# Kernel tuning notes

Measured on AMD Instinct MI355X. Metric: run time of the kernel, lower is better.

The kernel has to match this reference:

```python
import jax, jax.numpy as jnp
import numpy as np

N = 50000   # nodes
E = 800000  # edges
F = 128     # feat_dim
I = 128     # internal_dim
G = 64      # graphs in batch
EPS = 1e-5


def setup_inputs() -> dict:
    key = jax.random.key(0)
    ks = jax.random.split(key, 32)
    s = 0.1
    inp = {
        'x': jax.random.normal(ks[0], (N, F), dtype=jnp.float32),
        'edge_index': jax.random.randint(ks[1], (2, E), 0, N, dtype=jnp.int64),
        'batch': jnp.sort(jax.random.randint(ks[2], (N,), 0, G, dtype=jnp.int64)),
        # InitialSubnet: Linear(F->I) + BN(I)
        'init_W': jax.random.normal(ks[3], (F, I)) * s,
        'init_b': jnp.zeros((I,)),
        'init_g': jnp.ones((I,)),
        'init_bt': jnp.zeros((I,)),
        # 2 middle EdgeConv subnets: Linear(2I->I) + BN(I)
        'mid_W': jax.random.normal(ks[4], (2, 2 * I, I)) * s,
        'mid_b': jnp.zeros((2, I)),
        'mid_g': jnp.ones((2, I)),
        'mid_bt': jnp.zeros((2, I)),
        # 1 er / 1 pr receptor-specific EdgeConv subnet each
        'er_W': jax.random.normal(ks[5], (1, 2 * I, I)) * s,
        'er_b': jnp.zeros((1, I)),
        'er_g': jnp.ones((1, I)),
        'er_bt': jnp.zeros((1, I)),
        'pr_W': jax.random.normal(ks[6], (1, 2 * I, I)) * s,
        'pr_b': jnp.zeros((1, I)),
        'pr_g': jnp.ones((1, I)),
        'pr_bt': jnp.zeros((1, I)),
        # 3 shared posts: Linear(I->2) + BN(2)
        'spost_W': jax.random.normal(ks[7], (3, I, 2)) * s,
        'spost_b': jnp.zeros((3, 2)),
        'spost_g': jnp.ones((3, 2)),
        'spost_bt': jnp.zeros((3, 2)),
        # 1 er post / 1 pr post: Linear(I->1) + BN(1)
        'erpost_W': jax.random.normal(ks[8], (1, I, 1)) * s,
        'erpost_b': jnp.zeros((1, 1)),
        'erpost_g': jnp.ones((1, 1)),
        'erpost_bt': jnp.zeros((1, 1)),
        'prpost_W': jax.random.normal(ks[9], (1, I, 1)) * s,
        'prpost_b': jnp.zeros((1, 1)),
        'prpost_g': jnp.ones((1, 1)),
        'prpost_bt': jnp.zeros((1, 1)),
    }
    return inp


def _bn(h, g, b):
    # BatchNorm1d in training mode: batch stats over the row dim, biased var
    m = jnp.mean(h, axis=0)
    v = jnp.var(h, axis=0)
    return (h - m) * jax.lax.rsqrt(v + EPS) * g + b


def _edgeconv(h, src, dst, W, b, g, bt):
    # PyG EdgeConv: msg = nn(cat([x_i, x_j - x_i])), aggr=max over incoming edges
    x_i = h[dst]                      # [E, I]
    x_j = h[src]                      # [E, I]
    msg = jnp.concatenate([x_i, x_j - x_i], axis=-1) @ W + b  # [E, I]
    msg = jax.nn.elu(_bn(msg, g, bt))
    out = jax.ops.segment_max(msg, dst, num_segments=N)
    return jnp.where(jnp.isneginf(out), 0.0, out)  # isolated nodes -> 0


def _post(h, batch, counts, W, b, g, bt):
    # elu(BN(Linear(h))) then global_mean_pool; dropout is identity (eval)
    h2 = jax.nn.elu(_bn(h @ W + b, g, bt))
    pooled = jax.ops.segment_sum(h2, batch, num_segments=G)
    return pooled / counts[:, None]


def reference(x, edge_index, batch,
              init_W, init_b, init_g, init_bt,
              mid_W, mid_b, mid_g, mid_bt,
              er_W, er_b, er_g, er_bt,
              pr_W, pr_b, pr_g, pr_bt,
              spost_W, spost_b, spost_g, spost_bt,
              erpost_W, erpost_b, erpost_g, erpost_bt,
              prpost_W, prpost_b, prpost_g, prpost_bt):
    src, dst = edge_index[0], edge_index[1]
    counts = jnp.maximum(jax.ops.segment_sum(jnp.ones((N,), x.dtype), batch, num_segments=G), 1.0)

    outs = []
    # InitialSubnet: gelu(BN(Linear(x)))
    h = jax.nn.gelu(_bn(x @ init_W + init_b, init_g, init_bt), approximate=False)
    outs.append(_post(h, batch, counts, spost_W[0], spost_b[0], spost_g[0], spost_bt[0]))

    for l in range(2):
        h = _edgeconv(h, src, dst, mid_W[l], mid_b[l], mid_g[l], mid_bt[l])
        outs.append(_post(h, batch, counts, spost_W[l + 1], spost_b[l + 1], spost_g[l + 1], spost_bt[l + 1]))

    er_h = h
    pr_h = h
    for l in range(1):
        er_h = _edgeconv(er_h, src, dst, er_W[l], er_b[l], er_g[l], er_bt[l])
        er_out = _post(er_h, batch, counts, erpost_W[l], erpost_b[l], erpost_g[l], erpost_bt[l])
        pr_h = _edgeconv(pr_h, src, dst, pr_W[l], pr_b[l], pr_g[l], pr_bt[l])
        pr_out = _post(pr_h, batch, counts, prpost_W[l], prpost_b[l], prpost_g[l], prpost_bt[l])
        outs.append(jnp.concatenate([er_out, pr_out], axis=-1))

    agg = outs[0]
    for o in outs[1:]:
        agg = agg + o
    return agg  # [G, 2]
```

## Files before the change

### kernel.cpp

```cpp
#include <hip/hip_runtime.h>
#include <math.h>

#define EPS 1e-5f

typedef float f32x4v __attribute__((ext_vector_type(4)));
typedef short s16x8  __attribute__((ext_vector_type(8)));

__device__ __forceinline__ float elu_f(float x) { return x > 0.f ? x : expm1f(x); }
__device__ __forceinline__ float blo(unsigned u) { return __uint_as_float(u << 16); }
__device__ __forceinline__ float bhi(unsigned u) { return __uint_as_float(u & 0xffff0000u); }
__device__ __forceinline__ unsigned f2b(float f) {
  unsigned u = __float_as_uint(f);
  unsigned r = ((u >> 16) & 1u) + 0x7fffu;
  return (u + r) >> 16;
}
__device__ __forceinline__ unsigned pack2(float a, float b) {
  return f2b(a) | (f2b(b) << 16);
}

__global__ __launch_bounds__(256) void prep_csr0(const float* __restrict__ init_W,
    const float* __restrict__ mid_W, const float* __restrict__ er_W,
    const float* __restrict__ pr_W, const float* __restrict__ mid_g,
    const float* __restrict__ er_g, const float* __restrict__ pr_g,
    unsigned short* __restrict__ WT,
    const int* __restrict__ dst, int* __restrict__ partials, int Ecnt,
    const int* __restrict__ batch, float* __restrict__ counts, int Nn) {
  if (blockIdx.x < 320) {
    int grp = blockIdx.x >> 6;
    int i = (blockIdx.x & 63) * 256 + threadIdx.x;
    if (i >= 16384) return;
    int k = i >> 7, c = i & 127;
    if (grp == 0) {
      WT[c * 128 + k] = (unsigned short)f2b(init_W[k * 128 + c]);
      return;
    }
    const float* W; const float* g; unsigned short* Wd; unsigned short* W2;
    if (grp == 1)      { W = mid_W;             g = mid_g;       Wd = WT + 1 * 16384; W2 = WT + 2 * 16384; }
    else if (grp == 2) { W = mid_W + 256 * 128; g = mid_g + 128; Wd = WT + 3 * 16384; W2 = WT + 4 * 16384; }
    else if (grp == 3) { W = er_W;              g = er_g;        Wd = WT + 5 * 16384; W2 = WT + 6 * 16384; }
    else               { W = pr_W;              g = pr_g;        Wd = WT + 7 * 16384; W2 = WT + 8 * 16384; }
    float sg = (g[c] >= 0.f) ? 1.f : -1.f;
    float w1 = W[k * 128 + c];
    float w2 = W[(k + 128) * 128 + c];
    Wd[c * 128 + k] = (unsigned short)f2b((w1 - w2) * sg);
    W2[c * 128 + k] = (unsigned short)f2b(w2 * sg);
  } else {
    int b = blockIdx.x - 320;
    if (b < 64) {
      __shared__ int cnt[256];
      cnt[threadIdx.x] = 0;
      __syncthreads();
      int i0 = b * 256 + threadIdx.x, stride = 64 * 256;
      for (int e = i0; e < Ecnt; e += stride) atomicAdd(&cnt[(unsigned)dst[e] >> 8], 1);
      __syncthreads();
      partials[b * 256 + threadIdx.x] = cnt[threadIdx.x];
    } else {
      __shared__ float lc[64];
      if (threadIdx.x < 64) lc[threadIdx.x] = 0.f;
      __syncthreads();
      int i0 = (b - 64) * 256 + threadIdx.x, stride = 64 * 256;
      for (int n = i0; n < Nn; n += stride) atomicAdd(&lc[batch[n]], 1.f);
      __syncthreads();
      if (threadIdx.x < 64 && lc[threadIdx.x] != 0.f)
        atomicAdd(&counts[threadIdx.x * 16], lc[threadIdx.x]);
    }
  }
}

__global__ __launch_bounds__(256) void csr_p0_scan(const int* __restrict__ partials,
    int nblk, int* __restrict__ bucket_base, int* __restrict__ gcursor) {
  __shared__ int sc[256];
  int b = threadIdx.x;
  int s = 0;
  for (int k = 0; k < nblk; ++k) s += partials[k * 256 + b];
  sc[b] = s;
  __syncthreads();
  for (int off = 1; off < 256; off <<= 1) {
    int t = (b >= off) ? sc[b - off] : 0;
    __syncthreads();
    sc[b] += t;
    __syncthreads();
  }
  int excl = sc[b] - s;
  bucket_base[b] = excl;
  gcursor[b * 16] = excl;
  if (b == 255) bucket_base[256] = sc[255];
}

#define P1_CHUNK 4096
__global__ __launch_bounds__(256) void csr_p1_bin(const int* __restrict__ src,
    const int* __restrict__ dst, int* __restrict__ gcursor,
    unsigned* __restrict__ binned, int Ecnt) {
  __shared__ unsigned stage[P1_CHUNK];
  __shared__ int cnt[256], lbase[256], gbase[256], lcur[256], sc[256];
  int tid = threadIdx.x;
  int e0 = blockIdx.x * P1_CHUNK;
  int ecnt = Ecnt - e0; if (ecnt > P1_CHUNK) ecnt = P1_CHUNK;
  cnt[tid] = 0;
  __syncthreads();
  for (int i = tid; i < ecnt; i += 256) atomicAdd(&cnt[(unsigned)dst[e0 + i] >> 8], 1);
  __syncthreads();
  sc[tid] = cnt[tid];
  __syncthreads();
  for (int off = 1; off < 256; off <<= 1) {
    int t = (tid >= off) ? sc[tid - off] : 0;
    __syncthreads();
    sc[tid] += t;
    __syncthreads();
  }
  lbase[tid] = sc[tid] - cnt[tid];
  lcur[tid] = lbase[tid];
  gbase[tid] = (cnt[tid] > 0) ? atomicAdd(&gcursor[tid * 16], cnt[tid]) : 0;
  __syncthreads();
  for (int i = tid; i < ecnt; i += 256) {
    int d = dst[e0 + i], s = src[e0 + i];
    int bk = (unsigned)d >> 8;
    int p = atomicAdd(&lcur[bk], 1);
    stage[p] = ((unsigned)bk << 24) | ((unsigned)(d & 255) << 16) | (unsigned)s;
  }
  __syncthreads();
  for (int i = tid; i < ecnt; i += 256) {
    unsigned v = stage[i];
    int bk = v >> 24;
    binned[gbase[bk] + (i - lbase[bk])] = v;
  }
}

#define P2_CAP 12288
__global__ __launch_bounds__(256) void csr_p2_sort(const unsigned* __restrict__ binned,
    const int* __restrict__ bucket_base, unsigned short* __restrict__ csr_src,
    int* __restrict__ deg, int* __restrict__ rowstart, int Nn) {
  __shared__ unsigned short stage[P2_CAP];
  __shared__ int cnt[256], lbase[256], lcur[256], sc[256];
  int b = blockIdx.x, tid = threadIdx.x;
  int base = bucket_base[b];
  int bcnt = bucket_base[b + 1] - base;
  if (bcnt > P2_CAP) bcnt = P2_CAP;
  cnt[tid] = 0;
  __syncthreads();
  for (int i = tid; i < bcnt; i += 256) atomicAdd(&cnt[(binned[base + i] >> 16) & 255], 1);
  __syncthreads();
  sc[tid] = cnt[tid];
  __syncthreads();
  for (int off = 1; off < 256; off <<= 1) {
    int t = (tid >= off) ? sc[tid - off] : 0;
    __syncthreads();
    sc[tid] += t;
    __syncthreads();
  }
  lbase[tid] = sc[tid] - cnt[tid];
  lcur[tid] = lbase[tid];
  int node = b * 256 + tid;
  if (node < Nn) { deg[node] = cnt[tid]; rowstart[node] = base + lbase[tid]; }
  __syncthreads();
  for (int i = tid; i < bcnt; i += 256) {
    unsigned v = binned[base + i];
    int j = (v >> 16) & 255;
    int p = atomicAdd(&lcur[j], 1);
    stage[p] = (unsigned short)(v & 0xffffu);
  }
  __syncthreads();
  for (int i = tid; i < bcnt; i += 256) csr_src[base + i] = stage[i];
}

template<int XF32, int NMAT, int STATS>
__global__ __launch_bounds__(256, 3) void gemm_mfma(const void* __restrict__ Xv,
    const unsigned short* __restrict__ W0t, const unsigned short* __restrict__ W1t,
    const unsigned short* __restrict__ W2t, const unsigned short* __restrict__ W3t,
    unsigned short* __restrict__ Y0, unsigned short* __restrict__ Y1,
    unsigned short* __restrict__ Y2, unsigned short* __restrict__ Y3,
    float* __restrict__ stOut, int Nrows) {
  int tid = threadIdx.x, lane = tid & 63, wv = tid >> 6;
  int r0 = blockIdx.x * 64;
  int rlo = lane & 15, kg = lane >> 4;
  s16x8 zf = {0, 0, 0, 0, 0, 0, 0, 0};
  s16x8 af[4][4];
#pragma unroll
  for (int rg = 0; rg < 4; ++rg) {
    int arow = r0 + rg * 16 + rlo;
    if (arow < Nrows) {
      if (XF32) {
        const float* xr = (const float*)Xv + (size_t)arow * 128 + kg * 8;
#pragma unroll
        for (int s2 = 0; s2 < 4; ++s2) {
          float4 a = *(const float4*)(xr + s2 * 32);
          float4 b = *(const float4*)(xr + s2 * 32 + 4);
          s16x8 t;
          t[0] = (short)f2b(a.x); t[1] = (short)f2b(a.y);
          t[2] = (short)f2b(a.z); t[3] = (short)f2b(a.w);
          t[4] = (short)f2b(b.x); t[5] = (short)f2b(b.y);
          t[6] = (short)f2b(b.z); t[7] = (short)f2b(b.w);
          af[rg][s2] = t;
        }
      } else {
        const unsigned short* xr = (const unsigned short*)Xv + (size_t)arow * 128 + kg * 8;
#pragma unroll
        for (int s2 = 0; s2 < 4; ++s2) af[rg][s2] = *(const s16x8*)(xr + s2 * 32);
      }
    } else {
#pragma unroll
      for (int s2 = 0; s2 < 4; ++s2) af[rg][s2] = zf;
    }
  }
  const unsigned short* Ws[4] = {W0t, W1t, W2t, W3t};
  unsigned short* Ys[4] = {Y0, Y1, Y2, Y3};
#pragma unroll
  for (int o = 0; o < NMAT; ++o) {
    const unsigned short* Wt = Ws[o];
    unsigned short* Y = Ys[o];
#pragma unroll
    for (int t = 0; t < 2; ++t) {
      int nt = wv * 2 + t;
      const unsigned short* wp = Wt + (size_t)(nt * 16 + rlo) * 128 + kg * 8;
      s16x8 wf[4];
#pragma unroll
      for (int s2 = 0; s2 < 4; ++s2) wf[s2] = *(const s16x8*)(wp + s2 * 32);
      f32x4v acc[4];
#pragma unroll
      for (int rg = 0; rg < 4; ++rg) acc[rg] = (f32x4v){0.f, 0.f, 0.f, 0.f};
#pragma unroll
      for (int s2 = 0; s2 < 4; ++s2)
#pragma unroll
        for (int rg = 0; rg < 4; ++rg)
          acc[rg] = __builtin_amdgcn_mfma_f32_16x16x32_bf16(wf[s2], af[rg][s2], acc[rg], 0, 0, 0);
      float ps0 = 0.f, ps1 = 0.f, ps2 = 0.f, ps3 = 0.f;
      float pq0 = 0.f, pq1 = 0.f, pq2 = 0.f, pq3 = 0.f;
#pragma unroll
      for (int rg = 0; rg < 4; ++rg) {
        int arow = r0 + rg * 16 + rlo;
        if (arow < Nrows) {
          uint2 ov;
          ov.x = pack2(acc[rg][0], acc[rg][1]);
          ov.y = pack2(acc[rg][2], acc[rg][3]);
          *(uint2*)(Y + (size_t)arow * 128 + nt * 16 + kg * 4) = ov;
          if (STATS) {
            float y0 = blo(ov.x), y1 = bhi(ov.x), y2 = blo(ov.y), y3 = bhi(ov.y);
            ps0 += y0; pq0 += y0 * y0;
            ps1 += y1; pq1 += y1 * y1;
            ps2 += y2; pq2 += y2 * y2;
            ps3 += y3; pq3 += y3 * y3;
          }
        }
      }
      if (STATS) {
#pragma unroll
        for (int off = 1; off < 16; off <<= 1) {
          ps0 += __shfl_xor(ps0, off); pq0 += __shfl_xor(pq0, off);
          ps1 += __shfl_xor(ps1, off); pq1 += __shfl_xor(pq1, off);
          ps2 += __shfl_xor(ps2, off); pq2 += __shfl_xor(pq2, off);
          ps3 += __shfl_xor(ps3, off); pq3 += __shfl_xor(pq3, off);
        }
        if (rlo == 0) {
          int col = nt * 16 + kg * 4;
          float* sb = stOut + (size_t)(blockIdx.x & 15) * 256;
          atomicAdd(&sb[2 * col + 0], ps0); atomicAdd(&sb[2 * col + 1], pq0);
          atomicAdd(&sb[2 * (col + 1)], ps1); atomicAdd(&sb[2 * (col + 1) + 1], pq1);
          atomicAdd(&sb[2 * (col + 2)], ps2); atomicAdd(&sb[2 * (col + 2) + 1], pq2);
          atomicAdd(&sb[2 * (col + 3)], ps3); atomicAdd(&sb[2 * (col + 3) + 1], pq3);
        }
      }
    }
  }
}

__global__ __launch_bounds__(256, 8) void conv_pass(const unsigned short* __restrict__ A,
    const unsigned short* __restrict__ B, const unsigned short* __restrict__ csr_src,
    const int* __restrict__ rowstart, const int* __restrict__ deg,
    const float* __restrict__ g, unsigned short* __restrict__ Mx,
    float* __restrict__ st, int Nn, int convBlks,
    const float* __restrict__ zPp, const int* __restrict__ batch,
    const float* __restrict__ counts, const float* __restrict__ stpp,
    const float* __restrict__ g2, const float* __restrict__ bt2,
    float* __restrict__ out, float invN) {
  __shared__ float s_sum[128], s_ssq[128];
  int tid = threadIdx.x;
  if ((int)blockIdx.x >= convBlks) {
    __shared__ float lacc[128];
    if (tid < 128) lacc[tid] = 0.f;
    __syncthreads();
    float m0 = stpp[0] * invN, v0 = stpp[128] * invN - m0 * m0;
    float scale0 = g2[0] * rsqrtf(v0 + EPS), shift0 = bt2[0] - m0 * scale0;
    float m1 = stpp[64] * invN, v1 = stpp[192] * invN - m1 * m1;
    float scale1 = g2[1] * rsqrtf(v1 + EPS), shift1 = bt2[1] - m1 * scale1;
    int i0 = (blockIdx.x - convBlks) * 256 + tid;
    int stride = 32 * 256;
    for (int n = i0; n < Nn; n += stride) {
      int gi = batch[n];
      atomicAdd(&lacc[gi * 2], elu_f(zPp[n * 2] * scale0 + shift0));
      atomicAdd(&lacc[gi * 2 + 1], elu_f(zPp[n * 2 + 1] * scale1 + shift1));
    }
    __syncthreads();
    if (tid < 128) {
      int gi = tid >> 1, p = tid & 1;
      float v = lacc[tid];
      if (v != 0.f) atomicAdd(&out[gi * 2 + p], v / fmaxf(counts[gi * 16], 1.f));
    }
    return;
  }
  if (tid < 128) { s_sum[tid] = 0.f; s_ssq[tid] = 0.f; }
  __syncthreads();
  int lane = tid & 63;
  int wave = __builtin_amdgcn_readfirstlane((blockIdx.x << 2) + (tid >> 6));
  int wstride = convBlks << 2;
  int c0 = lane * 2;
  float sg0 = (g[c0] >= 0.f) ? 1.f : -1.f;
  float sg1 = (g[c0 + 1] >= 0.f) ? 1.f : -1.f;
  const unsigned* A32 = (const unsigned*)A;
  const unsigned* B32 = (const unsigned*)B;
  unsigned* M32 = (unsigned*)Mx;
  float s0 = 0.f, ss0 = 0.f, s1 = 0.f, ss1 = 0.f;
  for (int n = wave; n < Nn; n += wstride) {
    int dg = deg[n];
    if (dg == 0) continue;
    int beg = rowstart[n];
    unsigned ua = A32[(size_t)n * 64 + lane];
    float a0 = blo(ua), a1 = bhi(ua);
    float mx0 = -INFINITY, mx1 = -INFINITY;
    int e = beg, eend = beg + dg;
    for (; e + 8 <= eend; e += 8) {
      int idx[8];
#pragma unroll
      for (int q = 0; q < 8; ++q) idx[q] = csr_src[e + q];
      unsigned uu[8];
#pragma unroll
      for (int q = 0; q < 8; ++q) uu[q] = B32[(size_t)idx[q] * 64 + lane];
#pragma unroll
      for (int q = 0; q < 8; ++q) {
        float m0 = a0 + blo(uu[q]), m1 = a1 + bhi(uu[q]);
        s0 += m0; ss0 += m0 * m0;
        s1 += m1; ss1 += m1 * m1;
        mx0 = fmaxf(mx0, m0);
        mx1 = fmaxf(mx1, m1);
      }
    }
    for (; e + 2 <= eend; e += 2) {
      int ia = csr_src[e], ib = csr_src[e + 1];
      unsigned u0 = B32[(size_t)ia * 64 + lane];
      unsigned u1 = B32[(size_t)ib * 64 + lane];
      float m00 = a0 + blo(u0), m01 = a1 + bhi(u0);
      float m10 = a0 + blo(u1), m11 = a1 + bhi(u1);
      s0 += m00 + m10; ss0 += m00 * m00 + m10 * m10;
      s1 += m01 + m11; ss1 += m01 * m01 + m11 * m11;
      mx0 = fmaxf(mx0, fmaxf(m00, m10));
      mx1 = fmaxf(mx1, fmaxf(m01, m11));
    }
    if (e < eend) {
      unsigned u0 = B32[(size_t)csr_src[e] * 64 + lane];
      float m00 = a0 + blo(u0), m01 = a1 + bhi(u0);
      s0 += m00; ss0 += m00 * m00;
      s1 += m01; ss1 += m01 * m01;
      mx0 = fmaxf(mx0, m00);
      mx1 = fmaxf(mx1, m01);
    }
    M32[(size_t)n * 64 + lane] = pack2(mx0, mx1);
  }
  atomicAdd(&s_sum[c0], s0 * sg0); atomicAdd(&s_ssq[c0], ss0);
  atomicAdd(&s_sum[c0 + 1], s1 * sg1); atomicAdd(&s_ssq[c0 + 1], ss1);
  __syncthreads();
  if (tid < 128) {
    float* sb = st + (size_t)(blockIdx.x & 15) * 256;
    atomicAdd(&sb[2 * tid], s_sum[tid]);
    atomicAdd(&sb[2 * tid + 1], s_ssq[tid]);
  }
}

__global__ __launch_bounds__(256, 8) void conv_pass_dual(
    const unsigned short* __restrict__ Aer, const unsigned short* __restrict__ Ber,
    const unsigned short* __restrict__ Apr, const unsigned short* __restrict__ Bpr,
    const unsigned short* __restrict__ csr_src,
    const int* __restrict__ rowstart, const int* __restrict__ deg,
    const float* __restrict__ g_er, const float* __restrict__ g_pr,
    unsigned short* __restrict__ Mer, unsigned short* __restrict__ Mpr,
    float* __restrict__ st_er, float* __restrict__ st_pr, int Nn, int convBlks,
    const float* __restrict__ zPp, const int* __restrict__ batch,
    const float* __restrict__ counts, const float* __restrict__ stpp,
    const float* __restrict__ g2, const float* __restrict__ bt2,
    float* __restrict__ out, float invN) {
  __shared__ float s_e[256], s_p[256];
  int tid = threadIdx.x;
  if ((int)blockIdx.x >= convBlks) {
    __shared__ float lacc[128];
    if (tid < 128) lacc[tid] = 0.f;
    __syncthreads();
    float m0 = stpp[0] * invN, v0 = stpp[128] * invN - m0 * m0;
    float scale0 = g2[0] * rsqrtf(v0 + EPS), shift0 = bt2[0] - m0 * scale0;
    float m1 = stpp[64] * invN, v1 = stpp[192] * invN - m1 * m1;
    float scale1 = g2[1] * rsqrtf(v1 + EPS), shift1 = bt2[1] - m1 * scale1;
    int i0 = (blockIdx.x - convBlks) * 256 + tid;
    int stride = 32 * 256;
    for (int n = i0; n < Nn; n += stride) {
      int gi = batch[n];
      atomicAdd(&lacc[gi * 2], elu_f(zPp[n * 2] * scale0 + shift0));
      atomicAdd(&lacc[gi * 2 + 1], elu_f(zPp[n * 2 + 1] * scale1 + shift1));
    }
    __syncthreads();
    if (tid < 128) {
      int gi = tid >> 1, p = tid & 1;
      float v = lacc[tid];
      if (v != 0.f) atomicAdd(&out[gi * 2 + p], v / fmaxf(counts[gi * 16], 1.f));
    }
    return;
  }
  s_e[tid] = 0.f; s_p[tid] = 0.f;
  __syncthreads();
  int lane = tid & 63;
  int wave = __builtin_amdgcn_readfirstlane((blockIdx.x << 2) + (tid >> 6));
  int wstride = convBlks << 2;
  int c0 = lane * 2;
  float sge0 = (g_er[c0] >= 0.f) ? 1.f : -1.f;
  float sge1 = (g_er[c0 + 1] >= 0.f) ? 1.f : -1.f;
  float sgp0 = (g_pr[c0] >= 0.f) ? 1.f : -1.f;
  float sgp1 = (g_pr[c0 + 1] >= 0.f) ? 1.f : -1.f;
  const unsigned* Ae32 = (const unsigned*)Aer;
  const unsigned* Be32 = (const unsigned*)Ber;
  const unsigned* Ap32 = (const unsigned*)Apr;
  const unsigned* Bp32 = (const unsigned*)Bpr;
  unsigned* Me32 = (unsigned*)Mer;
  unsigned* Mp32 = (unsigned*)Mpr;
  float se0 = 0.f, sse0 = 0.f, se1 = 0.f, sse1 = 0.f;
  float sp0 = 0.f, ssp0 = 0.f, sp1 = 0.f, ssp1 = 0.f;
  for (int n = wave; n < Nn; n += wstride) {
    int dg = deg[n];
    if (dg == 0) continue;
    int beg = rowstart[n];
    unsigned uae = Ae32[(size_t)n * 64 + lane];
    unsigned uap = Ap32[(size_t)n * 64 + lane];
    float ae0 = blo(uae), ae1 = bhi(uae);
    float ap0 = blo(uap), ap1 = bhi(uap);
    float mxe0 = -INFINITY, mxe1 = -INFINITY, mxp0 = -INFINITY, mxp1 = -INFINITY;
    int e = beg, eend = beg + dg;
    for (; e + 8 <= eend; e += 8) {
      int idx[8];
#pragma unroll
      for (int q = 0; q < 8; ++q) idx[q] = csr_src[e + q];
      unsigned ue[8], up[8];
#pragma unroll
      for (int q = 0; q < 8; ++q) ue[q] = Be32[(size_t)idx[q] * 64 + lane];
#pragma unroll
      for (int q = 0; q < 8; ++q) up[q] = Bp32[(size_t)idx[q] * 64 + lane];
#pragma unroll
      for (int q = 0; q < 8; ++q) {
        float me0 = ae0 + blo(ue[q]), me1 = ae1 + bhi(ue[q]);
        float mp0 = ap0 + blo(up[q]), mp1 = ap1 + bhi(up[q]);
        se0 += me0; sse0 += me0 * me0; se1 += me1; sse1 += me1 * me1;
        sp0 += mp0; ssp0 += mp0 * mp0; sp1 += mp1; ssp1 += mp1 * mp1;
        mxe0 = fmaxf(mxe0, me0); mxe1 = fmaxf(mxe1, me1);
        mxp0 = fmaxf(mxp0, mp0); mxp1 = fmaxf(mxp1, mp1);
      }
    }
    for (; e + 2 <= eend; e += 2) {
      int i0 = csr_src[e], i1 = csr_src[e + 1];
      unsigned ue0 = Be32[(size_t)i0 * 64 + lane];
      unsigned up0 = Bp32[(size_t)i0 * 64 + lane];
      unsigned ue1 = Be32[(size_t)i1 * 64 + lane];
      unsigned up1 = Bp32[(size_t)i1 * 64 + lane];
      float me0 = ae0 + blo(ue0), me1 = ae1 + bhi(ue0);
      float mp0 = ap0 + blo(up0), mp1 = ap1 + bhi(up0);
      float ne0 = ae0 + blo(ue1), ne1 = ae1 + bhi(ue1);
      float np0 = ap0 + blo(up1), np1 = ap1 + bhi(up1);
      se0 += me0 + ne0; sse0 += me0 * me0 + ne0 * ne0;
      se1 += me1 + ne1; sse1 += me1 * me1 + ne1 * ne1;
      sp0 += mp0 + np0; ssp0 += mp0 * mp0 + np0 * np0;
      sp1 += mp1 + np1; ssp1 += mp1 * mp1 + np1 * np1;
      mxe0 = fmaxf(mxe0, fmaxf(me0, ne0)); mxe1 = fmaxf(mxe1, fmaxf(me1, ne1));
      mxp0 = fmaxf(mxp0, fmaxf(mp0, np0)); mxp1 = fmaxf(mxp1, fmaxf(mp1, np1));
    }
    if (e < eend) {
      int i0 = csr_src[e];
      unsigned ue = Be32[(size_t)i0 * 64 + lane];
      unsigned up = Bp32[(size_t)i0 * 64 + lane];
      float me0 = ae0 + blo(ue), me1 = ae1 + bhi(ue);
      float mp0 = ap0 + blo(up), mp1 = ap1 + bhi(up);
      se0 += me0; sse0 += me0 * me0; se1 += me1; sse1 += me1 * me1;
      sp0 += mp0; ssp0 += mp0 * mp0; sp1 += mp1; ssp1 += mp1 * mp1;
      mxe0 = fmaxf(mxe0, me0); mxe1 = fmaxf(mxe1, me1);
      mxp0 = fmaxf(mxp0, mp0); mxp1 = fmaxf(mxp1, mp1);
    }
    Me32[(size_t)n * 64 + lane] = pack2(mxe0, mxe1);
    Mp32[(size_t)n * 64 + lane] = pack2(mxp0, mxp1);
  }
  atomicAdd(&s_e[2 * c0], se0 * sge0);       atomicAdd(&s_e[2 * c0 + 1], sse0);
  atomicAdd(&s_e[2 * (c0 + 1)], se1 * sge1); atomicAdd(&s_e[2 * (c0 + 1) + 1], sse1);
  atomicAdd(&s_p[2 * c0], sp0 * sgp0);       atomicAdd(&s_p[2 * c0 + 1], ssp0);
  atomicAdd(&s_p[2 * (c0 + 1)], sp1 * sgp1); atomicAdd(&s_p[2 * (c0 + 1) + 1], ssp1);
  __syncthreads();
  {
    float* se = st_er + (size_t)(blockIdx.x & 15) * 256;
    float* sp = st_pr + (size_t)(blockIdx.x & 15) * 256;
    atomicAdd(&se[tid], s_e[tid]);
    atomicAdd(&sp[tid], s_p[tid]);
  }
}

template<int MODE>
__global__ __launch_bounds__(256) void fused_post16(const unsigned short* __restrict__ Zb,
    const int* __restrict__ deg, const float* __restrict__ stn,
    const float* __restrict__ g, const float* __restrict__ bt,
    const float* __restrict__ Wp, unsigned short* __restrict__ Hb,
    float* __restrict__ zP, float* __restrict__ stp, int Nn, float invCnt, int P) {
  __shared__ float lscale[128], lshift[128];
  __shared__ float red[4][4];
  int tid = threadIdx.x;
  if (tid < 128) {
    float sm = 0.f, sq = 0.f;
#pragma unroll
    for (int k = 0; k < 16; ++k) {
      sm += stn[k * 256 + 2 * tid];
      sq += stn[k * 256 + 2 * tid + 1];
    }
    float mean = sm * invCnt;
    float var = sq * invCnt - mean * mean;
    float sc = g[tid] * rsqrtf(var + EPS);
    float sh = bt[tid] - mean * sc;
    if (MODE == 1 && g[tid] < 0.f) sc = -sc;
    lscale[tid] = sc; lshift[tid] = sh;
  }
  __syncthreads();
  int sub = tid & 15, c0 = sub * 8;
  float sc[8], sh[8], w0[8], w1[8];
#pragma unroll
  for (int j = 0; j < 8; ++j) {
    sc[j] = lscale[c0 + j]; sh[j] = lshift[c0 + j];
    w0[j] = Wp[(c0 + j) * P];
    w1[j] = (P > 1) ? Wp[(c0 + j) * P + 1] : 0.f;
  }
  int g0 = (blockIdx.x * 256 + tid) >> 4;
  int gstride = gridDim.x * 16;
  bool leader = (sub == 0);
  float s0 = 0.f, ss0 = 0.f, s1 = 0.f, ss1 = 0.f;
  for (int n = g0; n < Nn; n += gstride) {
    float d0 = 0.f, d1 = 0.f;
    unsigned ow[4];
    bool live = (MODE == 0) || (deg[n] > 0);
    if (live) {
      uint4 v = ((const uint4*)(Zb + (size_t)n * 128))[sub];
      unsigned w[4] = {v.x, v.y, v.z, v.w};
#pragma unroll
      for (int u = 0; u < 4; ++u) {
        float t0 = blo(w[u]) * sc[2 * u] + sh[2 * u];
        float t1 = bhi(w[u]) * sc[2 * u + 1] + sh[2 * u + 1];
        float y0, y1;
        if (MODE == 0) {
          y0 = 0.5f * t0 * (1.f + erff(t0 * 0.70710678118f));
          y1 = 0.5f * t1 * (1.f + erff(t1 * 0.70710678118f));
        } else {
          y0 = elu_f(t0); y1 = elu_f(t1);
        }
        d0 += y0 * w0[2 * u] + y1 * w0[2 * u + 1];
        d1 += y0 * w1[2 * u] + y1 * w1[2 * u + 1];
        ow[u] = pack2(y0, y1);
      }
    } else {
      ow[0] = ow[1] = ow[2] = ow[3] = 0u;
    }
    if (Hb) ((uint4*)(Hb + (size_t)n * 128))[sub] = make_uint4(ow[0], ow[1], ow[2], ow[3]);
#pragma unroll
    for (int off = 1; off < 16; off <<= 1) {
      d0 += __shfl_xor(d0, off);
      d1 += __shfl_xor(d1, off);
    }
    if (leader) {
      zP[n * 2] = d0;
      if (P > 1) zP[n * 2 + 1] = d1;
      s0 += d0; ss0 += d0 * d0; s1 += d1; ss1 += d1 * d1;
    }
  }
  s0 += __shfl_xor(s0, 16);  s0 += __shfl_xor(s0, 32);
  s1 += __shfl_xor(s1, 16);  s1 += __shfl_xor(s1, 32);
  ss0 += __shfl_xor(ss0, 16); ss0 += __shfl_xor(ss0, 32);
  ss1 += __shfl_xor(ss1, 16); ss1 += __shfl_xor(ss1, 32);
  int wv = tid >> 6;
  if ((tid & 63) == 0) { red[wv][0] = s0; red[wv][1] = s1; red[wv][2] = ss0; red[wv][3] = ss1; }
  __syncthreads();
  if (tid < 4) {
    float v = red[0][tid] + red[1][tid] + red[2][tid] + red[3][tid];
    atomicAdd(&stp[tid * 64], v);
  }
}

__global__ __launch_bounds__(256) void fused_post16_dual(
    const unsigned short* __restrict__ Mer, const unsigned short* __restrict__ Mpr,
    const int* __restrict__ deg,
    const float* __restrict__ st_er, const float* __restrict__ st_pr,
    const float* __restrict__ g_er, const float* __restrict__ bt_er,
    const float* __restrict__ g_pr, const float* __restrict__ bt_pr,
    const float* __restrict__ Wer, const float* __restrict__ Wpr,
    float* __restrict__ zP, float* __restrict__ stp_er, float* __restrict__ stp_pr,
    int Nn, float invE) {
  __shared__ float sce_l[128], she_l[128], scp_l[128], shp_l[128];
  __shared__ float red[4][4];
  int tid = threadIdx.x;
  if (tid < 128) {
    float sme = 0.f, sqe = 0.f, smp = 0.f, sqp = 0.f;
#pragma unroll
    for (int k = 0; k < 16; ++k) {
      sme += st_er[k * 256 + 2 * tid];
      sqe += st_er[k * 256 + 2 * tid + 1];
      smp += st_pr[k * 256 + 2 * tid];
      sqp += st_pr[k * 256 + 2 * tid + 1];
    }
    float mean = sme * invE;
    float var = sqe * invE - mean * mean;
    float sc = g_er[tid] * rsqrtf(var + EPS);
    she_l[tid] = bt_er[tid] - mean * sc;
    sce_l[tid] = (g_er[tid] < 0.f) ? -sc : sc;
    mean = smp * invE;
    var = sqp * invE - mean * mean;
    sc = g_pr[tid] * rsqrtf(var + EPS);
    shp_l[tid] = bt_pr[tid] - mean * sc;
    scp_l[tid] = (g_pr[tid] < 0.f) ? -sc : sc;
  }
  __syncthreads();
  int sub = tid & 15, c0 = sub * 8;
  float sce[8], she[8], scp[8], shp[8], we[8], wp[8];
#pragma unroll
  for (int j = 0; j < 8; ++j) {
    sce[j] = sce_l[c0 + j]; she[j] = she_l[c0 + j];
    scp[j] = scp_l[c0 + j]; shp[j] = shp_l[c0 + j];
    we[j] = Wer[c0 + j]; wp[j] = Wpr[c0 + j];
  }
  int g0 = (blockIdx.x * 256 + tid) >> 4;
  int gstride = gridDim.x * 16;
  bool leader = (sub == 0);
  float s0 = 0.f, ss0 = 0.f, s1 = 0.f, ss1 = 0.f;
  for (int n = g0; n < Nn; n += gstride) {
    float d0 = 0.f, d1 = 0.f;
    if (deg[n] > 0) {
      uint4 ve = ((const uint4*)(Mer + (size_t)n * 128))[sub];
      uint4 vp = ((const uint4*)(Mpr + (size_t)n * 128))[sub];
      unsigned wea[4] = {ve.x, ve.y, ve.z, ve.w};
      unsigned wpa[4] = {vp.x, vp.y, vp.z, vp.w};
#pragma unroll
      for (int u = 0; u < 4; ++u) {
        float te0 = blo(wea[u]) * sce[2 * u] + she[2 * u];
        float te1 = bhi(wea[u]) * sce[2 * u + 1] + she[2 * u + 1];
        float tp0 = blo(wpa[u]) * scp[2 * u] + shp[2 * u];
        float tp1 = bhi(wpa[u]) * scp[2 * u + 1] + shp[2 * u + 1];
        d0 += elu_f(te0) * we[2 * u] + elu_f(te1) * we[2 * u + 1];
        d1 += elu_f(tp0) * wp[2 * u] + elu_f(tp1) * wp[2 * u + 1];
      }
    }
#pragma unroll
    for (int off = 1; off < 16; off <<= 1) {
      d0 += __shfl_xor(d0, off);
      d1 += __shfl_xor(d1, off);
    }
    if (leader) {
      zP[n * 2] = d0;
      zP[n * 2 + 1] = d1;
      s0 += d0; ss0 += d0 * d0; s1 += d1; ss1 += d1 * d1;
    }
  }
  s0 += __shfl_xor(s0, 16);  s0 += __shfl_xor(s0, 32);
  s1 += __shfl_xor(s1, 16);  s1 += __shfl_xor(s1, 32);
  ss0 += __shfl_xor(ss0, 16); ss0 += __shfl_xor(ss0, 32);
  ss1 += __shfl_xor(ss1, 16); ss1 += __shfl_xor(ss1, 32);
  int wv = tid >> 6;
  if ((tid & 63) == 0) { red[wv][0] = s0; red[wv][1] = s1; red[wv][2] = ss0; red[wv][3] = ss1; }
  __syncthreads();
  if (tid < 4) {
    float v = red[0][tid] + red[1][tid] + red[2][tid] + red[3][tid];
    if (tid == 0) atomicAdd(&stp_er[0], v);
    else if (tid == 1) atomicAdd(&stp_pr[0], v);
    else if (tid == 2) atomicAdd(&stp_er[128], v);
    else atomicAdd(&stp_pr[128], v);
  }
}

__global__ __launch_bounds__(256) void post_phase2_dual(const float* __restrict__ zP,
    const int* __restrict__ batch, const float* __restrict__ counts,
    const float* __restrict__ st_er, const float* __restrict__ st_pr,
    const float* __restrict__ g_er, const float* __restrict__ bt_er,
    const float* __restrict__ g_pr, const float* __restrict__ bt_pr,
    float* __restrict__ out, int Nrows, float invN) {
  __shared__ float lacc[128];
  if (threadIdx.x < 128) lacc[threadIdx.x] = 0.f;
  __syncthreads();
  float m0 = st_er[0] * invN;
  float v0 = st_er[128] * invN - m0 * m0;
  float scale0 = g_er[0] * rsqrtf(v0 + EPS);
  float shift0 = bt_er[0] - m0 * scale0;
  float m1 = st_pr[0] * invN;
  float v1 = st_pr[128] * invN - m1 * m1;
  float scale1 = g_pr[0] * rsqrtf(v1 + EPS);
  float shift1 = bt_pr[0] - m1 * scale1;
  int i0 = blockIdx.x * 256 + threadIdx.x;
  int stride = gridDim.x * 256;
  for (int n = i0; n < Nrows; n += stride) {
    int gi = batch[n];
    float y0 = elu_f(zP[n * 2] * scale0 + shift0);
    float y1 = elu_f(zP[n * 2 + 1] * scale1 + shift1);
    atomicAdd(&lacc[gi * 2], y0);
    atomicAdd(&lacc[gi * 2 + 1], y1);
  }
  __syncthreads();
  if (threadIdx.x < 128) {
    int gi = threadIdx.x >> 1, p = threadIdx.x & 1;
    float v = lacc[threadIdx.x];
    if (v != 0.f)
      atomicAdd(&out[gi * 2 + p], v / fmaxf(counts[gi * 16], 1.f));
  }
}

extern "C" void kernel_launch(void* const* d_in, const int* in_sizes, int n_in,
                              void* d_out, int out_size, void* d_ws, size_t ws_size,
                              hipStream_t stream) {
  const float* x       = (const float*)d_in[0];
  const int*   ei      = (const int*)d_in[1];
  const int*   batch   = (const int*)d_in[2];
  const float* init_W  = (const float*)d_in[3];
  const float* init_g  = (const float*)d_in[5];
  const float* init_bt = (const float*)d_in[6];
  const float* mid_W   = (const float*)d_in[7];
  const float* mid_g   = (const float*)d_in[9];
  const float* mid_bt  = (const float*)d_in[10];
  const float* er_W    = (const float*)d_in[11];
  const float* er_g    = (const float*)d_in[13];
  const float* er_bt   = (const float*)d_in[14];
  const float* pr_W    = (const float*)d_in[15];
  const float* pr_g    = (const float*)d_in[17];
  const float* pr_bt   = (const float*)d_in[18];
  const float* spost_W  = (const float*)d_in[19];
  const float* spost_g  = (const float*)d_in[21];
  const float* spost_bt = (const float*)d_in[22];
  const float* erpost_W  = (const float*)d_in[23];
  const float* erpost_g  = (const float*)d_in[25];
  const float* erpost_bt = (const float*)d_in[26];
  const float* prpost_W  = (const float*)d_in[27];
  const float* prpost_g  = (const float*)d_in[29];
  const float* prpost_bt = (const float*)d_in[30];

  int N = in_sizes[0] / 128;
  int E = in_sizes[1] / 2;
  float invN = 1.f / (float)N;
  float invE = 1.f / (float)E;
  float* out = (float*)d_out;

  const int CONV_BLKS = 2048;
  int nbuck = (N + 255) >> 8;

  size_t NB = (size_t)N * 128;
  unsigned short* Hb  = (unsigned short*)d_ws;
  unsigned short* Tb0 = Hb + NB;
  unsigned short* Tb1 = Tb0 + NB;
  unsigned short* Tb2 = Tb1 + NB;
  unsigned short* Tb3 = Tb2 + NB;
  unsigned short* MxB = Tb3 + NB;
  unsigned short* MxB2 = MxB + NB;
  float* zP     = (float*)(MxB2 + NB);
  float* counts = zP + (size_t)2 * N;
  float* stats  = counts + 1024;
  float* post   = stats + 5 * 4096;
  unsigned short* WT = (unsigned short*)(post + 5 * 512);
  int* deg        = (int*)(WT + 9 * 16384);
  int* rowstart   = deg + N;
  int* bucketbase = rowstart + N;
  int* gcursor    = bucketbase + 320;
  int* partials   = gcursor + 256 * 16;
  unsigned* binned = (unsigned*)(partials + 64 * 256);
  unsigned short* csr_src = (unsigned short*)(binned + E);

  int gemmGrid = (N + 63) / 64;

  hipMemsetAsync(d_out, 0, out_size * sizeof(float), stream);
  hipMemsetAsync(counts, 0, (1024 + 5 * 4096 + 5 * 512) * sizeof(float), stream);

  const int* e_src = ei;
  const int* e_dst = ei + E;
  prep_csr0<<<448, 256, 0, stream>>>(init_W, mid_W, er_W, pr_W, mid_g, er_g, pr_g, WT,
                                     e_dst, partials, E, batch, counts, N);
  csr_p0_scan<<<1, 256, 0, stream>>>(partials, 64, bucketbase, gcursor);
  csr_p1_bin<<<(E + P1_CHUNK - 1) / P1_CHUNK, 256, 0, stream>>>(e_src, e_dst, gcursor, binned, E);
  csr_p2_sort<<<nbuck, 256, 0, stream>>>(binned, bucketbase, csr_src, deg, rowstart, N);

  gemm_mfma<1, 1, 1><<<gemmGrid, 256, 0, stream>>>((const void*)x, WT, nullptr, nullptr, nullptr,
                                                   Tb0, nullptr, nullptr, nullptr, stats, N);
  fused_post16<0><<<512, 256, 0, stream>>>(Tb0, deg, stats, init_g, init_bt, spost_W,
                                           Hb, zP, post + 0 * 512, N, invN, 2);

  gemm_mfma<0, 2, 0><<<gemmGrid, 256, 0, stream>>>((const void*)Hb,
      WT + 1 * 16384, WT + 2 * 16384, nullptr, nullptr, Tb0, Tb1, nullptr, nullptr, nullptr, N);
  conv_pass<<<CONV_BLKS + 32, 256, 0, stream>>>(Tb0, Tb1, csr_src, rowstart, deg, mid_g,
      MxB, stats + 1 * 4096, N, CONV_BLKS,
      zP, batch, counts, post + 0 * 512, spost_g, spost_bt, out, invN);
  fused_post16<1><<<512, 256, 0, stream>>>(MxB, deg, stats + 1 * 4096, mid_g, mid_bt,
                                           spost_W + 256, Hb, zP, post + 1 * 512, N, invE, 2);

  gemm_mfma<0, 2, 0><<<gemmGrid, 256, 0, stream>>>((const void*)Hb,
      WT + 3 * 16384, WT + 4 * 16384, nullptr, nullptr, Tb0, Tb1, nullptr, nullptr, nullptr, N);
  conv_pass<<<CONV_BLKS + 32, 256, 0, stream>>>(Tb0, Tb1, csr_src, rowstart, deg, mid_g + 128,
      MxB, stats + 2 * 4096, N, CONV_BLKS,
      zP, batch, counts, post + 1 * 512, spost_g + 2, spost_bt + 2, out, invN);
  fused_post16<1><<<512, 256, 0, stream>>>(MxB, deg, stats + 2 * 4096, mid_g + 128, mid_bt + 128,
                                           spost_W + 512, Hb, zP, post + 2 * 512, N, invE, 2);

  gemm_mfma<0, 4, 0><<<gemmGrid, 256, 0, stream>>>((const void*)Hb,
      WT + 5 * 16384, WT + 6 * 16384, WT + 7 * 16384, WT + 8 * 16384,
      Tb0, Tb1, Tb2, Tb3, nullptr, N);
  conv_pass_dual<<<CONV_BLKS + 32, 256, 0, stream>>>(Tb0, Tb1, Tb2, Tb3, csr_src, rowstart, deg,
      er_g, pr_g, MxB, MxB2, stats + 3 * 4096, stats + 4 * 4096, N, CONV_BLKS,
      zP, batch, counts, post + 2 * 512, spost_g + 4, spost_bt + 4, out, invN);

  fused_post16_dual<<<512, 256, 0, stream>>>(MxB, MxB2, deg,
      stats + 3 * 4096, stats + 4 * 4096, er_g, er_bt, pr_g, pr_bt,
      erpost_W, prpost_W, zP, post + 3 * 512, post + 4 * 512, N, invE);
  post_phase2_dual<<<32, 256, 0, stream>>>(zP, batch, counts,
      post + 3 * 512, post + 4 * 512, erpost_g, erpost_bt, prpost_g, prpost_bt,
      out, N, invN);
}
```

Baseline: 419.8 us.

## Fuse BN+activation+post projection into the following MFMA GEMM prologue

Replaces the separate fused_post16 kernels and the following gemm_mfma with a single gemm_act kernel. It applies batch-norm, GELU/ELU and the post projection to each 64-row tile in shared memory, then runs the MFMA matmuls from LDS. The goal is to drop the write and re-read of the intermediate activation buffer Hb and to save kernel launches. In exchange, each GEMM block now does the activation work, and launch_bounds(256,3) with the larger LDS use may reduce occupancy.

New measurement: 385.5 us. 8.2% less time.

```diff
diff --git a/kernel.cpp b/kernel.cpp
--- a/kernel.cpp
+++ b/kernel.cpp
@@ -263,6 +263,133 @@
   }
 }
 
+template<int NMAT, int ACT>
+__global__ __launch_bounds__(256, 3) void gemm_act(const unsigned short* __restrict__ Xv,
+    const unsigned short* __restrict__ W0t, const unsigned short* __restrict__ W1t,
+    const unsigned short* __restrict__ W2t, const unsigned short* __restrict__ W3t,
+    unsigned short* __restrict__ Y0, unsigned short* __restrict__ Y1,
+    unsigned short* __restrict__ Y2, unsigned short* __restrict__ Y3,
+    const float* __restrict__ stn, const float* __restrict__ g,
+    const float* __restrict__ bt, const int* __restrict__ deg,
+    const float* __restrict__ Wp, float* __restrict__ zP, float* __restrict__ stp,
+    float invCnt, int Nrows) {
+  __shared__ unsigned short hl[64][136];
+  __shared__ float lsc[128], lsh[128], lw0[128], lw1[128];
+  __shared__ float red[4][4];
+  int tid = threadIdx.x, lane = tid & 63, wv = tid >> 6;
+  int r0 = blockIdx.x * 64;
+  int rlo = lane & 15, kg = lane >> 4;
+  if (tid < 128) {
+    float sm = 0.f, sq = 0.f;
+#pragma unroll
+    for (int k = 0; k < 16; ++k) {
+      sm += stn[k * 256 + 2 * tid];
+      sq += stn[k * 256 + 2 * tid + 1];
+    }
+    float mean = sm * invCnt;
+    float var = sq * invCnt - mean * mean;
+    float sc = g[tid] * rsqrtf(var + EPS);
+    float sh = bt[tid] - mean * sc;
+    if (ACT == 2 && g[tid] < 0.f) sc = -sc;
+    lsc[tid] = sc; lsh[tid] = sh;
+    lw0[tid] = Wp[tid * 2]; lw1[tid] = Wp[tid * 2 + 1];
+  }
+  __syncthreads();
+  {
+    int row = tid >> 2, q = tid & 3;
+    int arow = r0 + row;
+    bool rok = arow < Nrows;
+    int lrow = rok ? arow : 0;
+    float live = 1.f;
+    if (ACT == 2) live = (rok && deg[arow] > 0) ? 1.f : 0.f;
+    else live = rok ? 1.f : 0.f;
+    const uint4* xr = (const uint4*)(Xv + (size_t)lrow * 128 + q * 32);
+    float dd0 = 0.f, dd1 = 0.f;
+#pragma unroll
+    for (int b = 0; b < 4; ++b) {
+      uint4 v = xr[b];
+      unsigned w[4] = {v.x, v.y, v.z, v.w};
+      int cb = q * 32 + b * 8;
+#pragma unroll
+      for (int u = 0; u < 4; ++u) {
+        int c = cb + 2 * u;
+        float t0 = blo(w[u]) * lsc[c] + lsh[c];
+        float t1 = bhi(w[u]) * lsc[c + 1] + lsh[c + 1];
+        float y0, y1;
+        if (ACT == 1) {
+          y0 = 0.5f * t0 * (1.f + erff(t0 * 0.70710678118f));
+          y1 = 0.5f * t1 * (1.f + erff(t1 * 0.70710678118f));
+        } else {
+          y0 = elu_f(t0); y1 = elu_f(t1);
+        }
+        y0 *= live; y1 *= live;
+        *(unsigned*)&hl[row][c] = pack2(y0, y1);
+        dd0 += y0 * lw0[c] + y1 * lw0[c + 1];
+        dd1 += y0 * lw1[c] + y1 * lw1[c + 1];
+      }
+    }
+    dd0 += __shfl_xor(dd0, 1); dd0 += __shfl_xor(dd0, 2);
+    dd1 += __shfl_xor(dd1, 1); dd1 += __shfl_xor(dd1, 2);
+    if (q == 0 && rok) {
+      zP[(size_t)arow * 2] = dd0;
+      zP[(size_t)arow * 2 + 1] = dd1;
+    }
+    float s0v = (q == 0 && rok) ? dd0 : 0.f;
+    float s1v = (q == 0 && rok) ? dd1 : 0.f;
+    float q0v = s0v * s0v, q1v = s1v * s1v;
+#pragma unroll
+    for (int off = 4; off < 64; off <<= 1) {
+      s0v += __shfl_xor(s0v, off); s1v += __shfl_xor(s1v, off);
+      q0v += __shfl_xor(q0v, off); q1v += __shfl_xor(q1v, off);
+    }
+    if (lane == 0) { red[wv][0] = s0v; red[wv][1] = s1v; red[wv][2] = q0v; red[wv][3] = q1v; }
+  }
+  __syncthreads();
+  if (tid < 4) {
+    float v = red[0][tid] + red[1][tid] + red[2][tid] + red[3][tid];
+    atomicAdd(&stp[tid * 64], v);
+  }
+  s16x8 af[4][4];
+#pragma unroll
+  for (int rg = 0; rg < 4; ++rg)
+#pragma unroll
+    for (int s2 = 0; s2 < 4; ++s2)
+      af[rg][s2] = *(const s16x8*)&hl[rg * 16 + rlo][kg * 8 + s2 * 32];
+  const unsigned short* Ws[4] = {W0t, W1t, W2t, W3t};
+  unsigned short* Ys[4] = {Y0, Y1, Y2, Y3};
+#pragma unroll
+  for (int o = 0; o < NMAT; ++o) {
+    const unsigned short* Wt = Ws[o];
+    unsigned short* Y = Ys[o];
+#pragma unroll
+    for (int t = 0; t < 2; ++t) {
+      int nt = wv * 2 + t;
+      const unsigned short* wp = Wt + (size_t)(nt * 16 + rlo) * 128 + kg * 8;
+      s16x8 wf[4];
+#pragma unroll
+      for (int s2 = 0; s2 < 4; ++s2) wf[s2] = *(const s16x8*)(wp + s2 * 32);
+      f32x4v acc[4];
+#pragma unroll
+      for (int rg = 0; rg < 4; ++rg) acc[rg] = (f32x4v){0.f, 0.f, 0.f, 0.f};
+#pragma unroll
+      for (int s2 = 0; s2 < 4; ++s2)
+#pragma unroll
+        for (int rg = 0; rg < 4; ++rg)
+          acc[rg] = __builtin_amdgcn_mfma_f32_16x16x32_bf16(wf[s2], af[rg][s2], acc[rg], 0, 0, 0);
+#pragma unroll
+      for (int rg = 0; rg < 4; ++rg) {
+        int arow = r0 + rg * 16 + rlo;
+        if (arow < Nrows) {
+          uint2 ov;
+          ov.x = pack2(acc[rg][0], acc[rg][1]);
+          ov.y = pack2(acc[rg][2], acc[rg][3]);
+          *(uint2*)(Y + (size_t)arow * 128 + nt * 16 + kg * 4) = ov;
+        }
+      }
+    }
+  }
+}
+
 __global__ __launch_bounds__(256, 8) void conv_pass(const unsigned short* __restrict__ A,
     const unsigned short* __restrict__ B, const unsigned short* __restrict__ csr_src,
     const int* __restrict__ rowstart, const int* __restrict__ deg,
@@ -492,92 +619,6 @@
   }
 }
 
-template<int MODE>
-__global__ __launch_bounds__(256) void fused_post16(const unsigned short* __restrict__ Zb,
-    const int* __restrict__ deg, const float* __restrict__ stn,
-    const float* __restrict__ g, const float* __restrict__ bt,
-    const float* __restrict__ Wp, unsigned short* __restrict__ Hb,
-    float* __restrict__ zP, float* __restrict__ stp, int Nn, float invCnt, int P) {
-  __shared__ float lscale[128], lshift[128];
-  __shared__ float red[4][4];
-  int tid = threadIdx.x;
-  if (tid < 128) {
-    float sm = 0.f, sq = 0.f;
-#pragma unroll
-    for (int k = 0; k < 16; ++k) {
-      sm += stn[k * 256 + 2 * tid];
-      sq += stn[k * 256 + 2 * tid + 1];
-    }
-    float mean = sm * invCnt;
-    float var = sq * invCnt - mean * mean;
-    float sc = g[tid] * rsqrtf(var + EPS);
-    float sh = bt[tid] - mean * sc;
-    if (MODE == 1 && g[tid] < 0.f) sc = -sc;
-    lscale[tid] = sc; lshift[tid] = sh;
-  }
-  __syncthreads();
-  int sub = tid & 15, c0 = sub * 8;
-  float sc[8], sh[8], w0[8], w1[8];
-#pragma unroll
-  for (int j = 0; j < 8; ++j) {
-    sc[j] = lscale[c0 + j]; sh[j] = lshift[c0 + j];
-    w0[j] = Wp[(c0 + j) * P];
-    w1[j] = (P > 1) ? Wp[(c0 + j) * P + 1] : 0.f;
-  }
-  int g0 = (blockIdx.x * 256 + tid) >> 4;
-  int gstride = gridDim.x * 16;
-  bool leader = (sub == 0);
-  float s0 = 0.f, ss0 = 0.f, s1 = 0.f, ss1 = 0.f;
-  for (int n = g0; n < Nn; n += gstride) {
-    float d0 = 0.f, d1 = 0.f;
-    unsigned ow[4];
-    bool live = (MODE == 0) || (deg[n] > 0);
-    if (live) {
-      uint4 v = ((const uint4*)(Zb + (size_t)n * 128))[sub];
-      unsigned w[4] = {v.x, v.y, v.z, v.w};
-#pragma unroll
-      for (int u = 0; u < 4; ++u) {
-        float t0 = blo(w[u]) * sc[2 * u] + sh[2 * u];
-        float t1 = bhi(w[u]) * sc[2 * u + 1] + sh[2 * u + 1];
-        float y0, y1;
-        if (MODE == 0) {
-          y0 = 0.5f * t0 * (1.f + erff(t0 * 0.70710678118f));
-          y1 = 0.5f * t1 * (1.f + erff(t1 * 0.70710678118f));
-        } else {
-          y0 = elu_f(t0); y1 = elu_f(t1);
-        }
-        d0 += y0 * w0[2 * u] + y1 * w0[2 * u + 1];
-        d1 += y0 * w1[2 * u] + y1 * w1[2 * u + 1];
-        ow[u] = pack2(y0, y1);
-      }
-    } else {
-      ow[0] = ow[1] = ow[2] = ow[3] = 0u;
-    }
-    if (Hb) ((uint4*)(Hb + (size_t)n * 128))[sub] = make_uint4(ow[0], ow[1], ow[2], ow[3]);
-#pragma unroll
-    for (int off = 1; off < 16; off <<= 1) {
-      d0 += __shfl_xor(d0, off);
-      d1 += __shfl_xor(d1, off);
-    }
-    if (leader) {
-      zP[n * 2] = d0;
-      if (P > 1) zP[n * 2 + 1] = d1;
-      s0 += d0; ss0 += d0 * d0; s1 += d1; ss1 += d1 * d1;
-    }
-  }
-  s0 += __shfl_xor(s0, 16);  s0 += __shfl_xor(s0, 32);
-  s1 += __shfl_xor(s1, 16);  s1 += __shfl_xor(s1, 32);
-  ss0 += __shfl_xor(ss0, 16); ss0 += __shfl_xor(ss0, 32);
-  ss1 += __shfl_xor(ss1, 16); ss1 += __shfl_xor(ss1, 32);
-  int wv = tid >> 6;
-  if ((tid & 63) == 0) { red[wv][0] = s0; red[wv][1] = s1; red[wv][2] = ss0; red[wv][3] = ss1; }
-  __syncthreads();
-  if (tid < 4) {
-    float v = red[0][tid] + red[1][tid] + red[2][tid] + red[3][tid];
-    atomicAdd(&stp[tid * 64], v);
-  }
-}
-
 __global__ __launch_bounds__(256) void fused_post16_dual(
     const unsigned short* __restrict__ Mer, const unsigned short* __restrict__ Mpr,
     const int* __restrict__ deg,
@@ -740,8 +781,8 @@
   int nbuck = (N + 255) >> 8;
 
   size_t NB = (size_t)N * 128;
-  unsigned short* Hb  = (unsigned short*)d_ws;
-  unsigned short* Tb0 = Hb + NB;
+  unsigned short* TbI = (unsigned short*)d_ws;
+  unsigned short* Tb0 = TbI + NB;
   unsigned short* Tb1 = Tb0 + NB;
   unsigned short* Tb2 = Tb1 + NB;
   unsigned short* Tb3 = Tb2 + NB;
@@ -774,29 +815,30 @@
   csr_p2_sort<<<nbuck, 256, 0, stream>>>(binned, bucketbase, csr_src, deg, rowstart, N);
 
   gemm_mfma<1, 1, 1><<<gemmGrid, 256, 0, stream>>>((const void*)x, WT, nullptr, nullptr, nullptr,
-                                                   Tb0, nullptr, nullptr, nullptr, stats, N);
-  fused_post16<0><<<512, 256, 0, stream>>>(Tb0, deg, stats, init_g, init_bt, spost_W,
-                                           Hb, zP, post + 0 * 512, N, invN, 2);
-
-  gemm_mfma<0, 2, 0><<<gemmGrid, 256, 0, stream>>>((const void*)Hb,
-      WT + 1 * 16384, WT + 2 * 16384, nullptr, nullptr, Tb0, Tb1, nullptr, nullptr, nullptr, N);
+                                                   TbI, nullptr, nullptr, nullptr, stats, N);
+
+  gemm_act<2, 1><<<gemmGrid, 256, 0, stream>>>(TbI,
+      WT + 1 * 16384, WT + 2 * 16384, nullptr, nullptr, Tb0, Tb1, nullptr, nullptr,
+      stats, init_g, init_bt, deg, spost_W, zP, post + 0 * 512, invN, N);
+
   conv_pass<<<CONV_BLKS + 32, 256, 0, stream>>>(Tb0, Tb1, csr_src, rowstart, deg, mid_g,
       MxB, stats + 1 * 4096, N, CONV_BLKS,
       zP, batch, counts, post + 0 * 512, spost_g, spost_bt, out, invN);
-  fused_post16<1><<<512, 256, 0, stream>>>(MxB, deg, stats + 1 * 4096, mid_g, mid_bt,
-                                           spost_W + 256, Hb, zP, post + 1 * 512, N, invE, 2);
-
-  gemm_mfma<0, 2, 0><<<gemmGrid, 256, 0, stream>>>((const void*)Hb,
-      WT + 3 * 16384, WT + 4 * 16384, nullptr, nullptr, Tb0, Tb1, nullptr, nullptr, nullptr, N);
+
+  gemm_act<2, 2><<<gemmGrid, 256, 0, stream>>>(MxB,
+      WT + 3 * 16384, WT + 4 * 16384, nullptr, nullptr, Tb0, Tb1, nullptr, nullptr,
+      stats + 1 * 4096, mid_g, mid_bt, deg, spost_W + 256, zP, post + 1 * 512, invE, N);
+
   conv_pass<<<CONV_BLKS + 32, 256, 0, stream>>>(Tb0, Tb1, csr_src, rowstart, deg, mid_g + 128,
       MxB, stats + 2 * 4096, N, CONV_BLKS,
       zP, batch, counts, post + 1 * 512, spost_g + 2, spost_bt + 2, out, invN);
-  fused_post16<1><<<512, 256, 0, stream>>>(MxB, deg, stats + 2 * 4096, mid_g + 128, mid_bt + 128,
-                                           spost_W + 512, Hb, zP, post + 2 * 512, N, invE, 2);
-
-  gemm_mfma<0, 4, 0><<<gemmGrid, 256, 0, stream>>>((const void*)Hb,
+
+  gemm_act<4, 2><<<gemmGrid, 256, 0, stream>>>(MxB,
       WT + 5 * 16384, WT + 6 * 16384, WT + 7 * 16384, WT + 8 * 16384,
-      Tb0, Tb1, Tb2, Tb3, nullptr, N);
+      Tb0, Tb1, Tb2, Tb3,
+      stats + 2 * 4096, mid_g + 128, mid_bt + 128, deg, spost_W + 512,
+      zP, post + 2 * 512, invE, N);
+
   conv_pass_dual<<<CONV_BLKS + 32, 256, 0, stream>>>(Tb0, Tb1, Tb2, Tb3, csr_src, rowstart, deg,
       er_g, pr_g, MxB, MxB2, stats + 3 * 4096, stats + 4 * 4096, N, CONV_BLKS,
       zP, batch, counts, post + 2 * 512, spost_g + 4, spost_bt + 4, out, invN);
```
